# Kernel optimization log

Hardware: AMD Instinct MI355X
Metric: run time of the kernel (lower is better)

Reference implementation:

```python
import jax, jax.numpy as jnp
import numpy as np

EPS = 1e-5

def _conv1x1(x, w, b):
    # x: (b,c,h,w), w: (o,c) -> (b,o,h,w)
    return jnp.einsum('bchw,oc->bohw', x, w) + b[None, :, None, None]

def _maxpool2(x):
    b, c, h, w = x.shape
    return x.reshape(b, c, h // 2, 2, w // 2, 2).max(axis=(3, 5))

def setup_inputs() -> dict:
    key = jax.random.key(0)
    ks = jax.random.split(key, 11)
    C, CI, H, W, B = 256, 128, 64, 64, 8
    s = 0.05
    return {
        'x': jax.random.normal(ks[0], (B, C, H, W), jnp.float32),
        'Wg': jax.random.normal(ks[1], (CI, C), jnp.float32) * s,
        'bg': jax.random.normal(ks[2], (CI,), jnp.float32) * s,
        'Wt': jax.random.normal(ks[3], (CI, C), jnp.float32) * s,
        'bt': jax.random.normal(ks[4], (CI,), jnp.float32) * s,
        'Wp': jax.random.normal(ks[5], (CI, C), jnp.float32) * s,
        'bp': jax.random.normal(ks[6], (CI,), jnp.float32) * s,
        'Ww': jax.random.normal(ks[7], (C, CI), jnp.float32) * s,
        'bw': jax.random.normal(ks[8], (C,), jnp.float32) * s,
        'gamma': jax.random.normal(ks[9], (C,), jnp.float32),
        'beta': jax.random.normal(ks[10], (C,), jnp.float32),
    }

def reference(x, Wg, bg, Wt, bt, Wp, bp, Ww, bw, gamma, beta):
    b, C, H, W = x.shape
    CI = Wg.shape[0]
    # g and phi are sub-sampled by 2x2 max pool -> M = (H/2)*(W/2); theta keeps N = H*W
    g_x = _maxpool2(_conv1x1(x, Wg, bg)).reshape(b, CI, -1).transpose(0, 2, 1)   # (b,M,ci)
    theta_x = _conv1x1(x, Wt, bt).reshape(b, CI, -1).transpose(0, 2, 1)          # (b,N,ci)
    phi_x = _maxpool2(_conv1x1(x, Wp, bp)).reshape(b, CI, -1)                    # (b,ci,M)
    f = jnp.einsum('bnc,bcm->bnm', theta_x, phi_x)                               # (b,N,M)
    f_div_C = jax.nn.softmax(f, axis=-1)
    y = jnp.einsum('bnm,bmc->bnc', f_div_C, g_x)                                 # (b,N,ci)
    y = y.transpose(0, 2, 1).reshape(b, CI, H, W)
    # W: 1x1 conv + BatchNorm2d (training mode: batch statistics, biased var)
    wy = _conv1x1(y, Ww, bw)
    mean = wy.mean(axis=(0, 2, 3), keepdims=True)
    var = ((wy - mean) ** 2).mean(axis=(0, 2, 3), keepdims=True)
    wy = (wy - mean) * jax.lax.rsqrt(var + EPS)
    wy = wy * gamma[None, :, None, None] + beta[None, :, None, None]
    z = wy + x
    # self.avg_pool is AdaptiveMaxPool2d(1): global spatial max
    return z.max(axis=(2, 3), keepdims=True)
```

## Files before the change

kernel.cpp:

```cpp
#include <hip/hip_runtime.h>
#include <hip/hip_bf16.h>
#include <stdint.h>

using f32x4  = __attribute__((ext_vector_type(4))) float;
using bf16x8 = __attribute__((ext_vector_type(8))) short;
using short4v = __attribute__((ext_vector_type(4))) short;

#define DEVINL static __device__ __forceinline__

DEVINL short f2bf(float f) {
    union { float f; uint32_t u; } v; v.f = f;
    uint32_t r = (v.u + 0x7FFFu + ((v.u >> 16) & 1u)) >> 16;
    return (short)(uint16_t)r;
}
DEVINL float bf2f(short s) {
    union { uint32_t u; float f; } v; v.u = ((uint32_t)(uint16_t)s) << 16;
    return v.f;
}
DEVINL float fexp2(float x) {
    float r;
    asm("v_exp_f32 %0, %1" : "=v"(r) : "v"(x));
    return r;
}
DEVINL uint32_t pk2bf(float a, float b) {
    union { __hip_bfloat162 v; uint32_t u; } c;
    c.v = __float22bfloat162_rn(float2{a, b});
    return c.u;
}

DEVINL void gld16(const short* g, short* l) {
    __builtin_amdgcn_global_load_lds(
        (const __attribute__((address_space(1))) unsigned int*)g,
        (__attribute__((address_space(3))) unsigned int*)l, 16, 0, 0);
}

#define LOG2E 1.44269504f

__global__ __launch_bounds__(256) void k0_prep(
        const float* __restrict__ Wg, const float* __restrict__ Wt, const float* __restrict__ Wp,
        const float* __restrict__ bg, const float* __restrict__ bt, const float* __restrict__ bp,
        const float* __restrict__ Ww,
        short* __restrict__ W_all, short* __restrict__ Ww16, float* __restrict__ b_all) {
    int i = blockIdx.x * 256 + threadIdx.x;
    if (i < 384 * 256) {
        int r = i >> 8, c = i & 255;
        float v = (r < 128) ? Wg[r * 256 + c]
                : (r < 256) ? Wt[(r - 128) * 256 + c] * LOG2E
                            : Wp[(r - 256) * 256 + c];
        W_all[i] = f2bf(v);
    } else if (i < 384 * 256 + 256 * 128) {
        int j = i - 384 * 256;
        Ww16[j] = f2bf(Ww[j]);
    }
    if (i < 384) {
        b_all[i] = (i < 128) ? bg[i] : (i < 256) ? bt[i - 128] * LOG2E : bp[i - 256];
    }
}

__global__ __launch_bounds__(256) void k1_conv(const float* __restrict__ x,
        const short* __restrict__ W_all, const float* __restrict__ b_all,
        short* __restrict__ OutT, short* __restrict__ Kmat, short* __restrict__ Vmat) {
    __shared__ short xs[128 * 32];
    __shared__ short obuf[128 * 128];
    const int ntile = blockIdx.x;
    const int otile = blockIdx.y;
    const int b     = blockIdx.z;
    const int tid  = threadIdx.x;
    const int lane = tid & 63;
    const int wave = tid >> 6;
    const int wn = wave >> 1, wo = wave & 1;
    const int l15 = lane & 15, lh = lane >> 4;

    f32x4 acc[4][4];
    #pragma unroll
    for (int i = 0; i < 4; i++)
        #pragma unroll
        for (int j = 0; j < 4; j++) acc[i][j] = f32x4{0.f, 0.f, 0.f, 0.f};

    const int n0 = ntile * 128;
    const int ob = otile * 128 + wo * 64;
    const float* xb = x + (size_t)b * 256 * 4096;

    const int srow_base = (lane & 15) + wave * 16;
    const int sc0 = (lane >> 4) * 8;

    for (int kt = 0; kt < 8; kt++) {
        __syncthreads();
        #pragma unroll
        for (int p = 0; p < 2; p++) {
            int row = srow_base + p * 64;
            const float* xp = xb + (size_t)(kt * 32 + sc0) * 4096 + n0 + row;
            bf16x8 w8;
            #pragma unroll
            for (int j = 0; j < 8; j++) w8[j] = f2bf(xp[(size_t)j * 4096]);
            int ch = (sc0 >> 3) ^ ((row >> 1) & 3);
            *(bf16x8*)&xs[row * 32 + ch * 8] = w8;
        }
        __syncthreads();

        bf16x8 a[4], w[4];
        #pragma unroll
        for (int nf = 0; nf < 4; nf++) {
            int row = wn * 64 + nf * 16 + l15;
            int ch  = lh ^ ((row >> 1) & 3);
            a[nf] = *(const bf16x8*)&xs[row * 32 + ch * 8];
        }
        #pragma unroll
        for (int of = 0; of < 4; of++)
            w[of] = *(const bf16x8*)(W_all + (size_t)(ob + of * 16 + l15) * 256 + kt * 32 + lh * 8);
        #pragma unroll
        for (int nf = 0; nf < 4; nf++)
            #pragma unroll
            for (int of = 0; of < 4; of++)
                acc[nf][of] = __builtin_amdgcn_mfma_f32_16x16x32_bf16(a[nf], w[of], acc[nf][of], 0, 0, 0);
    }

    #pragma unroll
    for (int of = 0; of < 4; of++) {
        int ocol = wo * 64 + of * 16 + l15;
        float bias = b_all[otile * 128 + ocol];
        #pragma unroll
        for (int nf = 0; nf < 4; nf++)
            #pragma unroll
            for (int r = 0; r < 4; r++) {
                int n  = wn * 64 + nf * 16 + lh * 4 + r;
                int ch = (ocol >> 3) ^ (n & 15);
                obuf[n * 128 + ch * 8 + (ocol & 7)] = f2bf(acc[nf][of][r] + bias);
            }
    }
    __syncthreads();

    if (otile == 1) {
        #pragma unroll
        for (int p = 0; p < 8; p++) {
            int n  = wave * 4 + lh + p * 16;
            int ch = l15 ^ (n & 15);
            bf16x8 v = *(const bf16x8*)&obuf[n * 128 + ch * 8];
            *(bf16x8*)(OutT + ((size_t)b * 4096 + n0 + n) * 128 + l15 * 8) = v;
        }
    } else if (otile == 2) {
        const int wp = tid >> 3;
        const int cc = (tid & 7) * 16;
        short* kdst = Kmat + ((size_t)b * 1024 + ntile * 32 + wp) * 128 + cc;
        #pragma unroll
        for (int cblk = 0; cblk < 2; cblk++) {
            const int chunk = (cc >> 3) + cblk;
            float mx[8];
            #pragma unroll
            for (int j = 0; j < 8; j++) mx[j] = -1e30f;
            #pragma unroll
            for (int q4 = 0; q4 < 4; q4++) {
                int n = (q4 >> 1) * 64 + 2 * wp + (q4 & 1);
                bf16x8 v = *(const bf16x8*)&obuf[n * 128 + ((chunk ^ (n & 15)) * 8)];
                #pragma unroll
                for (int j = 0; j < 8; j++) mx[j] = fmaxf(mx[j], bf2f(v[j]));
            }
            bf16x8 vo;
            #pragma unroll
            for (int j = 0; j < 8; j++) vo[j] = f2bf(mx[j]);
            *(bf16x8*)(kdst + cblk * 8) = vo;
        }
    } else {
        const int c   = tid >> 1;
        const int wp0 = (tid & 1) * 16;
        const int chb = c >> 3, cl = c & 7;
        #pragma unroll
        for (int half = 0; half < 2; half++) {
            bf16x8 vo;
            #pragma unroll
            for (int j = 0; j < 8; j++) {
                int wp = wp0 + half * 8 + j;
                float mx = -1e30f;
                #pragma unroll
                for (int q4 = 0; q4 < 4; q4++) {
                    int n = (q4 >> 1) * 64 + 2 * wp + (q4 & 1);
                    mx = fmaxf(mx, bf2f(obuf[n * 128 + ((chb ^ (n & 15)) * 8) + cl]));
                }
                vo[j] = f2bf(mx);
            }
            *(bf16x8*)(Vmat + ((size_t)b * 128 + c) * 1024 + ntile * 32 + wp0 + half * 8) = vo;
        }
    }
}

__global__ __launch_bounds__(256) void k3_attn(const short* __restrict__ OutT,
        const short* __restrict__ Kmat, const short* __restrict__ Vmat,
        const short* __restrict__ Ww16, const float* __restrict__ bw,
        short* __restrict__ wy) {
    __shared__ short smem[36864];
    short* const sKb = smem;
    short* const sVb = smem + 16384;
    short* const sPb = smem + 32768;

    const int bid = blockIdx.x;
    const int b   = bid & 7;
    const int nt  = bid >> 3;
    const int tid = threadIdx.x;
    const int lane = tid & 63;
    const int wave = tid >> 6;
    const int l15 = lane & 15, lh = lane >> 4;
    const int nblk = nt * 64;
    const int n0 = nblk + wave * 16;

    const short* Kb = Kmat + (size_t)b * 1024 * 128;
    const short* Vb = Vmat + (size_t)b * 128 * 1024;
    short* sPw = sPb + wave * 1024;

    auto STAGE = [&](int t, int bufi) {
        const int m0 = t * 64;
        #pragma unroll
        for (int i = 0; i < 4; i++) {
            const int segb = (i * 4 + wave) * 64;
            const int rowK = (segb >> 4) + (lane >> 4);
            const int chkK = lane & 15;
            gld16(Kb + (size_t)(m0 + rowK) * 128 + ((chkK ^ (rowK & 15)) << 3),
                  sKb + bufi * 8192 + segb * 8);
            const int rowV = (segb >> 3) + (lane >> 3);
            const int chkV = lane & 7;
            gld16(Vb + (size_t)rowV * 1024 + m0 + ((chkV ^ (rowV & 7)) << 3),
                  sVb + bufi * 8192 + segb * 8);
        }
    };

    bf16x8 q[4];
    {
        const short* qrow = OutT + ((size_t)b * 4096 + n0 + l15) * 128;
        #pragma unroll
        for (int ks = 0; ks < 4; ks++)
            q[ks] = *(const bf16x8*)(qrow + ks * 32 + lh * 8);
    }

    f32x4 y[8];
    #pragma unroll
    for (int cf = 0; cf < 8; cf++) y[cf] = f32x4{0.f, 0.f, 0.f, 0.f};
    float mrun = -1e30f, lrun = 0.f;

    STAGE(0, 0);
    int cur = 0;

    for (int t = 0; t < 16; t++) {
        if (t < 15) {
            STAGE(t + 1, cur ^ 1);
            asm volatile("s_waitcnt vmcnt(8)" ::: "memory");
        } else {
            asm volatile("s_waitcnt vmcnt(0)" ::: "memory");
        }
        __builtin_amdgcn_s_barrier();
        __builtin_amdgcn_sched_barrier(0);

        const short* cK = sKb + cur * 8192;
        const short* cV = sVb + cur * 8192;

        f32x4 S[4];
        #pragma unroll
        for (int mf = 0; mf < 4; mf++) S[mf] = f32x4{0.f, 0.f, 0.f, 0.f};
        #pragma unroll
        for (int ks = 0; ks < 4; ks++) {
            bf16x8 kf[4];
            #pragma unroll
            for (int mf = 0; mf < 4; mf++) {
                int mrow = mf * 16 + l15;
                int jj   = ks * 4 + lh;
                kf[mf] = *(const bf16x8*)&cK[mrow * 128 + ((jj ^ (mrow & 15)) << 3)];
            }
            __builtin_amdgcn_s_setprio(1);
            #pragma unroll
            for (int mf = 0; mf < 4; mf++)
                S[mf] = __builtin_amdgcn_mfma_f32_16x16x32_bf16(kf[mf], q[ks], S[mf], 0, 0, 0);
            __builtin_amdgcn_s_setprio(0);
        }

        float pm = S[0][0];
        #pragma unroll
        for (int mf = 0; mf < 4; mf++)
            #pragma unroll
            for (int r = 0; r < 4; r++) pm = fmaxf(pm, S[mf][r]);
        pm = fmaxf(pm, __shfl_xor(pm, 16));
        pm = fmaxf(pm, __shfl_xor(pm, 32));

        if (__any(pm > mrun + 8.656f)) {
            float mnew  = fmaxf(mrun, pm);
            float alpha = fexp2(mrun - mnew);
            mrun = mnew;
            lrun *= alpha;
            float aR[4];
            #pragma unroll
            for (int r = 0; r < 4; r++) aR[r] = __shfl(alpha, lh * 4 + r);
            #pragma unroll
            for (int cf = 0; cf < 8; cf++)
                #pragma unroll
                for (int r = 0; r < 4; r++) y[cf][r] *= aR[r];
        }
        float rs = 0.f;
        #pragma unroll
        for (int mf = 0; mf < 4; mf++)
            #pragma unroll
            for (int r = 0; r < 4; r++) {
                float p = fexp2(S[mf][r] - mrun);
                S[mf][r] = p;
                rs += p;
            }
        rs += __shfl_xor(rs, 16);
        rs += __shfl_xor(rs, 32);
        lrun += rs;

        #pragma unroll
        for (int mf = 0; mf < 4; mf++) {
            uint2 pk = { pk2bf(S[mf][0], S[mf][1]), pk2bf(S[mf][2], S[mf][3]) };
            *(uint2*)&sPw[(l15 << 6) + (((mf * 4 + lh) ^ l15) << 2)] = pk;
        }

        #pragma unroll
        for (int ks2 = 0; ks2 < 2; ks2++) {
            int u0 = ks2 * 8 + lh * 2;
            short4v lo = *(const short4v*)&sPw[(l15 << 6) + (((u0)     ^ l15) << 2)];
            short4v hi = *(const short4v*)&sPw[(l15 << 6) + (((u0 + 1) ^ l15) << 2)];
            bf16x8 pa = { lo.x, lo.y, lo.z, lo.w, hi.x, hi.y, hi.z, hi.w };
            int jj = ks2 * 4 + lh;
            __builtin_amdgcn_s_setprio(1);
            #pragma unroll
            for (int cf = 0; cf < 8; cf++) {
                int crow = cf * 16 + l15;
                bf16x8 vf = *(const bf16x8*)&cV[crow * 64 + ((jj ^ (crow & 7)) << 3)];
                y[cf] = __builtin_amdgcn_mfma_f32_16x16x32_bf16(pa, vf, y[cf], 0, 0, 0);
            }
            __builtin_amdgcn_s_setprio(0);
        }

        __builtin_amdgcn_sched_barrier(0);
        __builtin_amdgcn_s_barrier();
        cur ^= 1;
    }

    float linv[4];
    #pragma unroll
    for (int r = 0; r < 4; r++) linv[r] = 1.f / __shfl(lrun, lh * 4 + r);

    short* const Yt = smem;
    #pragma unroll
    for (int cf = 0; cf < 8; cf++) {
        int c = cf * 16 + l15;
        #pragma unroll
        for (int r = 0; r < 4; r++) {
            int n = wave * 16 + lh * 4 + r;
            Yt[n * 128 + (((c >> 3) ^ (n & 15)) << 3) + (c & 7)] = f2bf(y[cf][r] * linv[r]);
        }
    }
    __syncthreads();

    bf16x8 by[4][4];
    #pragma unroll
    for (int nf = 0; nf < 4; nf++)
        #pragma unroll
        for (int ks = 0; ks < 4; ks++) {
            int n  = nf * 16 + l15;
            int kc = ks * 4 + lh;
            by[nf][ks] = *(const bf16x8*)&Yt[n * 128 + ((kc ^ (n & 15)) << 3)];
        }

    short* const sOut = smem + 8192 + wave * 4608;
    const int obase = wave * 64;
    #pragma unroll
    for (int of = 0; of < 4; of++) {
        bf16x8 aw[4];
        #pragma unroll
        for (int ks = 0; ks < 4; ks++)
            aw[ks] = *(const bf16x8*)(Ww16 + (size_t)(obase + of * 16 + l15) * 128 + ks * 32 + lh * 8);
        #pragma unroll
        for (int nf = 0; nf < 4; nf++) {
            f32x4 acc = f32x4{0.f, 0.f, 0.f, 0.f};
            #pragma unroll
            for (int ks = 0; ks < 4; ks++)
                acc = __builtin_amdgcn_mfma_f32_16x16x32_bf16(aw[ks], by[nf][ks], acc, 0, 0, 0);
            #pragma unroll
            for (int r = 0; r < 4; r++) {
                int o_loc = of * 16 + lh * 4 + r;
                sOut[o_loc * 72 + nf * 16 + l15] = f2bf(acc[r] + bw[obase + o_loc]);
            }
        }
    }

    #pragma unroll
    for (int p = 0; p < 8; p++) {
        int o_loc = p * 8 + (lane >> 3);
        int n8    = (lane & 7) * 8;
        bf16x8 v = *(const bf16x8*)&sOut[o_loc * 72 + n8];
        *(bf16x8*)(wy + ((size_t)b * 256 + obase + o_loc) * 4096 + nblk + n8) = v;
    }
}

__global__ __launch_bounds__(256) void k4s_stats(const short* __restrict__ wy,
        float* __restrict__ stats) {
    const int o = blockIdx.x;
    const int tid = threadIdx.x;
    float s = 0.f, s2 = 0.f;
    #pragma unroll
    for (int b = 0; b < 8; b++) {
        const short* p = wy + ((size_t)b * 256 + o) * 4096;
        #pragma unroll
        for (int i = 0; i < 2; i++) {
            bf16x8 v = *(const bf16x8*)(p + (tid + i * 256) * 8);
            #pragma unroll
            for (int j = 0; j < 8; j++) {
                float f = bf2f(v[j]);
                s += f; s2 += f * f;
            }
        }
    }
    #pragma unroll
    for (int off = 1; off < 64; off <<= 1) { s += __shfl_xor(s, off); s2 += __shfl_xor(s2, off); }
    __shared__ float red[4][2];
    if ((tid & 63) == 0) { red[tid >> 6][0] = s; red[tid >> 6][1] = s2; }
    __syncthreads();
    if (tid == 0) {
        stats[o * 2]     = red[0][0] + red[1][0] + red[2][0] + red[3][0];
        stats[o * 2 + 1] = red[0][1] + red[1][1] + red[2][1] + red[3][1];
    }
}

__global__ __launch_bounds__(256) void k5_bnmax(const short* __restrict__ wy,
        const float* __restrict__ x, const float* __restrict__ stats,
        const float* __restrict__ gamma, const float* __restrict__ beta,
        float* __restrict__ outp) {
    int b = blockIdx.x >> 8;
    int o = blockIdx.x & 255;
    int tid = threadIdx.x;
    float mean = stats[o * 2] * (1.f / 32768.f);
    float var  = stats[o * 2 + 1] * (1.f / 32768.f) - mean * mean;
    float rstd = rsqrtf(var + 1e-5f);
    float A = rstd * gamma[o];
    float B = beta[o] - mean * A;
    const short* pw = wy + ((size_t)b * 256 + o) * 4096;
    const float* px = x + ((size_t)b * 256 + o) * 4096;
    float mx = -1e30f;
    #pragma unroll
    for (int j = 0; j < 2; j++) {
        int e = (tid + j * 256) * 8;
        bf16x8 w8 = *(const bf16x8*)(pw + e);
        float4 xa = *(const float4*)(px + e);
        float4 xb = *(const float4*)(px + e + 4);
        mx = fmaxf(mx, bf2f(w8[0]) * A + B + xa.x);
        mx = fmaxf(mx, bf2f(w8[1]) * A + B + xa.y);
        mx = fmaxf(mx, bf2f(w8[2]) * A + B + xa.z);
        mx = fmaxf(mx, bf2f(w8[3]) * A + B + xa.w);
        mx = fmaxf(mx, bf2f(w8[4]) * A + B + xb.x);
        mx = fmaxf(mx, bf2f(w8[5]) * A + B + xb.y);
        mx = fmaxf(mx, bf2f(w8[6]) * A + B + xb.z);
        mx = fmaxf(mx, bf2f(w8[7]) * A + B + xb.w);
    }
    #pragma unroll
    for (int off = 1; off < 64; off <<= 1) mx = fmaxf(mx, __shfl_xor(mx, off));
    __shared__ float red[4];
    if ((tid & 63) == 0) red[tid >> 6] = mx;
    __syncthreads();
    if (tid == 0)
        outp[b * 256 + o] = fmaxf(fmaxf(red[0], red[1]), fmaxf(red[2], red[3]));
}

extern "C" void kernel_launch(void* const* d_in, const int* in_sizes, int n_in,
                              void* d_out, int out_size, void* d_ws, size_t ws_size,
                              hipStream_t stream) {
    const float* x     = (const float*)d_in[0];
    const float* Wg    = (const float*)d_in[1];
    const float* bg    = (const float*)d_in[2];
    const float* Wt    = (const float*)d_in[3];
    const float* bt    = (const float*)d_in[4];
    const float* Wp    = (const float*)d_in[5];
    const float* bp    = (const float*)d_in[6];
    const float* Ww    = (const float*)d_in[7];
    const float* bw    = (const float*)d_in[8];
    const float* gamma = (const float*)d_in[9];
    const float* beta  = (const float*)d_in[10];
    float* outp = (float*)d_out;

    char* ws = (char*)d_ws;
    size_t off = 0;
    auto alloc = [&](size_t bytes) -> void* {
        void* p = ws + off;
        off = (off + bytes + 255) & ~(size_t)255;
        return p;
    };
    short* W_all = (short*)alloc((size_t)384 * 256 * 2);
    short* Ww16  = (short*)alloc((size_t)256 * 128 * 2);
    float* b_all = (float*)alloc((size_t)384 * 4);
    short* OutT  = (short*)alloc((size_t)8 * 4096 * 128 * 2);
    short* Kmat  = (short*)alloc((size_t)8 * 1024 * 128 * 2);
    short* Vmat  = (short*)alloc((size_t)8 * 128 * 1024 * 2);
    short* wy    = (short*)alloc((size_t)8 * 256 * 4096 * 2);
    float* stats = (float*)alloc((size_t)256 * 2 * 4);

    k0_prep<<<512, 256, 0, stream>>>(Wg, Wt, Wp, bg, bt, bp, Ww, W_all, Ww16, b_all);
    k1_conv<<<dim3(32, 3, 8), 256, 0, stream>>>(x, W_all, b_all, OutT, Kmat, Vmat);
    k3_attn<<<512, 256, 0, stream>>>(OutT, Kmat, Vmat, Ww16, bw, wy);
    k4s_stats<<<256, 256, 0, stream>>>(wy, stats);
    k5_bnmax<<<2048, 256, 0, stream>>>(wy, x, stats, gamma, beta, outp);
}
```

Measured before the change: 88.05 us.

## Split attention KV range across two wave groups with final softmax merge

Doubles the attention block to 512 threads. Each half of the block processes half of the M keys, using 32-key tiles with new LDS layouts and swizzles. The two halves merge their partial flash-attention states (max, sum, accumulators) through shared memory before the output projection, which is now split across 8 waves. This is meant to add more waves for latency hiding. In exchange it adds a merge step, extra barriers, and smaller per-iteration MFMA batches.

```diff
diff --git a/kernel.cpp b/kernel.cpp
--- a/kernel.cpp
+++ b/kernel.cpp
@@ -183,14 +183,11 @@
     }
 }
 
-__global__ __launch_bounds__(256) void k3_attn(const short* __restrict__ OutT,
+__global__ __launch_bounds__(512, 4) void k3_attn(const short* __restrict__ OutT,
         const short* __restrict__ Kmat, const short* __restrict__ Vmat,
         const short* __restrict__ Ww16, const float* __restrict__ bw,
         short* __restrict__ wy) {
     __shared__ short smem[36864];
-    short* const sKb = smem;
-    short* const sVb = smem + 16384;
-    short* const sPb = smem + 32768;
 
     const int bid = blockIdx.x;
     const int b   = bid & 7;
@@ -198,27 +195,33 @@
     const int tid = threadIdx.x;
     const int lane = tid & 63;
     const int wave = tid >> 6;
+    const int half = wave >> 2;
+    const int wl   = wave & 3;
     const int l15 = lane & 15, lh = lane >> 4;
     const int nblk = nt * 64;
-    const int n0 = nblk + wave * 16;
+    const int n0 = nblk + wl * 16;
+    const int mbase = half * 512;
 
     const short* Kb = Kmat + (size_t)b * 1024 * 128;
     const short* Vb = Vmat + (size_t)b * 128 * 1024;
-    short* sPw = sPb + wave * 1024;
+    short* const sKh = smem + half * 8192;
+    short* const sVh = smem + 16384 + half * 8192;
+    short* const sPw = smem + 32768 + wave * 512;
 
     auto STAGE = [&](int t, int bufi) {
-        const int m0 = t * 64;
-        #pragma unroll
-        for (int i = 0; i < 4; i++) {
-            const int segb = (i * 4 + wave) * 64;
+        const int m0 = mbase + t * 32;
+        #pragma unroll
+        for (int i = 0; i < 2; i++) {
+            const int segb = (i * 4 + wl) * 64;
             const int rowK = (segb >> 4) + (lane >> 4);
             const int chkK = lane & 15;
             gld16(Kb + (size_t)(m0 + rowK) * 128 + ((chkK ^ (rowK & 15)) << 3),
-                  sKb + bufi * 8192 + segb * 8);
-            const int rowV = (segb >> 3) + (lane >> 3);
-            const int chkV = lane & 7;
-            gld16(Vb + (size_t)rowV * 1024 + m0 + ((chkV ^ (rowV & 7)) << 3),
-                  sVb + bufi * 8192 + segb * 8);
+                  sKh + bufi * 4096 + segb * 8);
+            const int rowV = (segb >> 2) + (lane >> 2);
+            const int chkV = lane & 3;
+            const int swzV = chkV ^ (rowV & 3) ^ ((rowV >> 2) & 3);
+            gld16(Vb + (size_t)rowV * 1024 + m0 + (swzV << 3),
+                  sVh + bufi * 4096 + segb * 8);
         }
     };
 
@@ -241,38 +244,38 @@
     for (int t = 0; t < 16; t++) {
         if (t < 15) {
             STAGE(t + 1, cur ^ 1);
-            asm volatile("s_waitcnt vmcnt(8)" ::: "memory");
+            asm volatile("s_waitcnt vmcnt(4)" ::: "memory");
         } else {
             asm volatile("s_waitcnt vmcnt(0)" ::: "memory");
         }
         __builtin_amdgcn_s_barrier();
         __builtin_amdgcn_sched_barrier(0);
 
-        const short* cK = sKb + cur * 8192;
-        const short* cV = sVb + cur * 8192;
-
-        f32x4 S[4];
-        #pragma unroll
-        for (int mf = 0; mf < 4; mf++) S[mf] = f32x4{0.f, 0.f, 0.f, 0.f};
+        const short* cK = sKh + cur * 4096;
+        const short* cV = sVh + cur * 4096;
+
+        f32x4 S[2];
+        #pragma unroll
+        for (int mf = 0; mf < 2; mf++) S[mf] = f32x4{0.f, 0.f, 0.f, 0.f};
         #pragma unroll
         for (int ks = 0; ks < 4; ks++) {
-            bf16x8 kf[4];
-            #pragma unroll
-            for (int mf = 0; mf < 4; mf++) {
+            bf16x8 kf[2];
+            #pragma unroll
+            for (int mf = 0; mf < 2; mf++) {
                 int mrow = mf * 16 + l15;
                 int jj   = ks * 4 + lh;
                 kf[mf] = *(const bf16x8*)&cK[mrow * 128 + ((jj ^ (mrow & 15)) << 3)];
             }
             __builtin_amdgcn_s_setprio(1);
             #pragma unroll
-            for (int mf = 0; mf < 4; mf++)
+            for (int mf = 0; mf < 2; mf++)
                 S[mf] = __builtin_amdgcn_mfma_f32_16x16x32_bf16(kf[mf], q[ks], S[mf], 0, 0, 0);
             __builtin_amdgcn_s_setprio(0);
         }
 
         float pm = S[0][0];
         #pragma unroll
-        for (int mf = 0; mf < 4; mf++)
+        for (int mf = 0; mf < 2; mf++)
             #pragma unroll
             for (int r = 0; r < 4; r++) pm = fmaxf(pm, S[mf][r]);
         pm = fmaxf(pm, __shfl_xor(pm, 16));
@@ -293,7 +296,7 @@
         }
         float rs = 0.f;
         #pragma unroll
-        for (int mf = 0; mf < 4; mf++)
+        for (int mf = 0; mf < 2; mf++)
             #pragma unroll
             for (int r = 0; r < 4; r++) {
                 float p = fexp2(S[mf][r] - mrun);
@@ -305,23 +308,22 @@
         lrun += rs;
 
         #pragma unroll
-        for (int mf = 0; mf < 4; mf++) {
+        for (int mf = 0; mf < 2; mf++) {
             uint2 pk = { pk2bf(S[mf][0], S[mf][1]), pk2bf(S[mf][2], S[mf][3]) };
-            *(uint2*)&sPw[(l15 << 6) + (((mf * 4 + lh) ^ l15) << 2)] = pk;
-        }
-
-        #pragma unroll
-        for (int ks2 = 0; ks2 < 2; ks2++) {
-            int u0 = ks2 * 8 + lh * 2;
-            short4v lo = *(const short4v*)&sPw[(l15 << 6) + (((u0)     ^ l15) << 2)];
-            short4v hi = *(const short4v*)&sPw[(l15 << 6) + (((u0 + 1) ^ l15) << 2)];
+            int cm = mf * 4 + lh;
+            *(uint2*)&sPw[(l15 << 5) + ((cm ^ (l15 & 7)) << 2)] = pk;
+        }
+
+        {
+            short4v lo = *(const short4v*)&sPw[(l15 << 5) + (((2 * lh)     ^ (l15 & 7)) << 2)];
+            short4v hi = *(const short4v*)&sPw[(l15 << 5) + (((2 * lh + 1) ^ (l15 & 7)) << 2)];
             bf16x8 pa = { lo.x, lo.y, lo.z, lo.w, hi.x, hi.y, hi.z, hi.w };
-            int jj = ks2 * 4 + lh;
             __builtin_amdgcn_s_setprio(1);
             #pragma unroll
             for (int cf = 0; cf < 8; cf++) {
                 int crow = cf * 16 + l15;
-                bf16x8 vf = *(const bf16x8*)&cV[crow * 64 + ((jj ^ (crow & 7)) << 3)];
+                int swz = lh ^ (crow & 3) ^ ((crow >> 2) & 3);
+                bf16x8 vf = *(const bf16x8*)&cV[crow * 32 + (swz << 3)];
                 y[cf] = __builtin_amdgcn_mfma_f32_16x16x32_bf16(pa, vf, y[cf], 0, 0, 0);
             }
             __builtin_amdgcn_s_setprio(0);
@@ -332,18 +334,54 @@
         cur ^= 1;
     }
 
-    float linv[4];
-    #pragma unroll
-    for (int r = 0; r < 4; r++) linv[r] = 1.f / __shfl(lrun, lh * 4 + r);
+    float* fsm = (float*)smem;
+    const int fbase = wl * 2080;
+    if (half == 1) {
+        #pragma unroll
+        for (int cf = 0; cf < 8; cf++)
+            #pragma unroll
+            for (int r = 0; r < 4; r++)
+                fsm[fbase + (lh * 4 + r) * 128 + cf * 16 + l15] = y[cf][r];
+        if (lh == 0) {
+            fsm[fbase + 2048 + l15] = lrun;
+            fsm[fbase + 2064 + l15] = mrun;
+        }
+    }
+    __syncthreads();
+    if (half == 0) {
+        float m1 = fsm[fbase + 2064 + l15];
+        float l1 = fsm[fbase + 2048 + l15];
+        float mnew = fmaxf(mrun, m1);
+        float a0 = fexp2(mrun - mnew);
+        float a1 = fexp2(m1 - mnew);
+        float lnew = lrun * a0 + l1 * a1;
+        float aR0[4], aR1[4], linv[4];
+        #pragma unroll
+        for (int r = 0; r < 4; r++) {
+            aR0[r] = __shfl(a0, lh * 4 + r);
+            aR1[r] = __shfl(a1, lh * 4 + r);
+            linv[r] = 1.f / __shfl(lnew, lh * 4 + r);
+        }
+        #pragma unroll
+        for (int cf = 0; cf < 8; cf++)
+            #pragma unroll
+            for (int r = 0; r < 4; r++) {
+                float y1 = fsm[fbase + (lh * 4 + r) * 128 + cf * 16 + l15];
+                y[cf][r] = (y[cf][r] * aR0[r] + y1 * aR1[r]) * linv[r];
+            }
+    }
+    __syncthreads();
 
     short* const Yt = smem;
-    #pragma unroll
-    for (int cf = 0; cf < 8; cf++) {
-        int c = cf * 16 + l15;
-        #pragma unroll
-        for (int r = 0; r < 4; r++) {
-            int n = wave * 16 + lh * 4 + r;
-            Yt[n * 128 + (((c >> 3) ^ (n & 15)) << 3) + (c & 7)] = f2bf(y[cf][r] * linv[r]);
+    if (half == 0) {
+        #pragma unroll
+        for (int cf = 0; cf < 8; cf++) {
+            int c = cf * 16 + l15;
+            #pragma unroll
+            for (int r = 0; r < 4; r++) {
+                int n = wl * 16 + lh * 4 + r;
+                Yt[n * 128 + (((c >> 3) ^ (n & 15)) << 3) + (c & 7)] = f2bf(y[cf][r]);
+            }
         }
     }
     __syncthreads();
@@ -358,10 +396,10 @@
             by[nf][ks] = *(const bf16x8*)&Yt[n * 128 + ((kc ^ (n & 15)) << 3)];
         }
 
-    short* const sOut = smem + 8192 + wave * 4608;
-    const int obase = wave * 64;
-    #pragma unroll
-    for (int of = 0; of < 4; of++) {
+    short* const sOut = smem + 8192 + wave * 2304;
+    const int obase = wave * 32;
+    #pragma unroll
+    for (int of = 0; of < 2; of++) {
         bf16x8 aw[4];
         #pragma unroll
         for (int ks = 0; ks < 4; ks++)
@@ -381,7 +419,7 @@
     }
 
     #pragma unroll
-    for (int p = 0; p < 8; p++) {
+    for (int p = 0; p < 4; p++) {
         int o_loc = p * 8 + (lane >> 3);
         int n8    = (lane & 7) * 8;
         bf16x8 v = *(const bf16x8*)&sOut[o_loc * 72 + n8];
@@ -491,7 +529,7 @@
 
     k0_prep<<<512, 256, 0, stream>>>(Wg, Wt, Wp, bg, bt, bp, Ww, W_all, Ww16, b_all);
     k1_conv<<<dim3(32, 3, 8), 256, 0, stream>>>(x, W_all, b_all, OutT, Kmat, Vmat);
-    k3_attn<<<512, 256, 0, stream>>>(OutT, Kmat, Vmat, Ww16, bw, wy);
+    k3_attn<<<512, 512, 0, stream>>>(OutT, Kmat, Vmat, Ww16, bw, wy);
     k4s_stats<<<256, 256, 0, stream>>>(wy, stats);
     k5_bnmax<<<2048, 256, 0, stream>>>(wy, x, stats, gamma, beta, outp);
 }
```

Result: no change. 88.89 us (+1.0%).
